# Optimization experiments

Hardware: AMD Instinct MI355X
Metric: run time of the kernel (lower is better)

## Reference

```python
import jax, jax.numpy as jnp
import numpy as np


def setup_inputs() -> dict:
    key = jax.random.key(0)
    k1, k2 = jax.random.split(key)
    B, N, M, D = 4, 8192, 8192, 3
    prediction = jax.random.normal(k1, (B, N, D), dtype=jnp.float32)
    target = jax.random.normal(k2, (B, M, D), dtype=jnp.float32)
    return {"prediction": prediction, "target": target}


def reference(prediction, target):
    # prediction: [B, N, 3], target: [B, M, 3] (already channels-last,
    # matching the module's transpose-if-needed behavior).
    x2 = jnp.sum(prediction * prediction, axis=-1)  # [B, N]
    y2 = jnp.sum(target * target, axis=-1)          # [B, M]
    xy = jnp.einsum('bnd,bmd->bnm', prediction, target)  # [B, N, M]
    d2 = x2[:, :, None] + y2[:, None, :] - 2.0 * xy
    d2 = jnp.maximum(d2, 0.0)  # numerical guard
    # pytorch3d chamfer_distance defaults: point_reduction='mean',
    # batch_reduction='mean' -> mean over points per direction, mean over batch,
    # then sum the two directions.
    cham_x = jnp.min(d2, axis=2).mean()  # pred -> target
    cham_y = jnp.min(d2, axis=1).mean()  # target -> pred
    return cham_x + cham_y
```

## Files before the change

kernel.cpp:

```cpp
#include <hip/hip_runtime.h>


#define BLOCK 256
#define RPT   8
#define MC    512
#define NPTS  8192
#define NCH   (NPTS / MC)
#define NB    4

__global__ __launch_bounds__(BLOCK) void chamfer_min_fused(
    const float* __restrict__ pred, const float* __restrict__ targ,
    float* __restrict__ pA,
    float* __restrict__ pB,
    double* __restrict__ acc, unsigned int* __restrict__ counter) {
    if (blockIdx.x == 0 && blockIdx.y == 0 && blockIdx.z == 0 && threadIdx.x == 0) {
        *acc = 0.0;
        *counter = 0u;
    }

    const int z   = blockIdx.z;
    const int dir = z >> 2, b = z & (NB - 1);
    const float* X = dir ? targ : pred;
    const float* Y = dir ? pred : targ;
    float* partial = dir ? pB : pA;

    __shared__ float4 ldsY[MC];
    const int mc = blockIdx.y;

    for (int p = threadIdx.x; p < MC; p += BLOCK) {
        const float* yp = Y + ((size_t)b * NPTS + (size_t)mc * MC + p) * 3;
        float yx = yp[0], yy = yp[1], yz = yp[2];
        ldsY[p] = make_float4(yx, yy, yz, fmaf(yx, yx, fmaf(yy, yy, yz * yz)));
    }
    __syncthreads();

    const int row0 = blockIdx.x * (BLOCK * RPT);
    float qx[RPT], qy[RPT], qz[RPT], x2[RPT], best[RPT];
#pragma unroll
    for (int r = 0; r < RPT; ++r) {
        int row = row0 + r * BLOCK + threadIdx.x;
        const float* xp = X + ((size_t)b * NPTS + row) * 3;
        float px = xp[0], py = xp[1], pz = xp[2];
        qx[r] = -2.0f * px;
        qy[r] = -2.0f * py;
        qz[r] = -2.0f * pz;
        x2[r] = fmaf(px, px, fmaf(py, py, pz * pz));
        best[r] = 3.0e38f;
    }

#pragma unroll 4
    for (int m = 0; m < MC; m += 2) {
        float4 T0 = ldsY[m];
        float4 T1 = ldsY[m + 1];
#pragma unroll
        for (int r = 0; r < RPT; ++r) {
            float c0 = fmaf(qx[r], T0.x, fmaf(qy[r], T0.y, fmaf(qz[r], T0.z, T0.w)));
            float c1 = fmaf(qx[r], T1.x, fmaf(qy[r], T1.y, fmaf(qz[r], T1.z, T1.w)));
            best[r] = fminf(fminf(best[r], c0), c1);
        }
    }

#pragma unroll
    for (int r = 0; r < RPT; ++r) {
        int row = row0 + r * BLOCK + threadIdx.x;
        partial[((size_t)b * NCH + mc) * NPTS + row] = fmaxf(best[r] + x2[r], 0.0f);
    }
}

__global__ __launch_bounds__(256) void chamfer_reduce(
    const float* __restrict__ pA, const float* __restrict__ pB,
    double* __restrict__ acc, unsigned int* __restrict__ counter,
    float* __restrict__ out) {
    const int g = blockIdx.x * 256 + threadIdx.x;
    const int half = NB * NPTS;
    const float* src = (g < half) ? pA : pB;
    const int gg = g & (half - 1);
    const int b = gg >> 13, r = gg & (NPTS - 1);

    float v = 3.0e38f;
#pragma unroll
    for (int c = 0; c < NCH; ++c)
        v = fminf(v, src[((size_t)b * NCH + c) * NPTS + r]);

    double d = (double)v;
    for (int off = 32; off > 0; off >>= 1) d += __shfl_down(d, off);
    __shared__ double sh[4];
    const int lane = threadIdx.x & 63, wid = threadIdx.x >> 6;
    if (lane == 0) sh[wid] = d;
    __syncthreads();

    if (threadIdx.x == 0) {
        double blocktotal = sh[0] + sh[1] + sh[2] + sh[3];
        atomicAdd(acc, blocktotal);
        __threadfence();
        unsigned int ticket = atomicAdd(counter, 1u);
        if (ticket == gridDim.x - 1) {
            __threadfence();
            double s = atomicAdd(acc, 0.0);
            out[0] = (float)(s / (double)(NB * NPTS));
        }
    }
}

extern "C" void kernel_launch(void* const* d_in, const int* in_sizes, int n_in,
                              void* d_out, int out_size, void* d_ws, size_t ws_size,
                              hipStream_t stream) {
    const float* pred = (const float*)d_in[0];
    const float* targ = (const float*)d_in[1];
    float* out = (float*)d_out;

    float* pA = (float*)d_ws;
    float* pB = pA + (size_t)NB * NCH * NPTS;
    double* acc = (double*)(pB + (size_t)NB * NCH * NPTS);
    unsigned int* counter = (unsigned int*)(acc + 1);

    dim3 g1(NPTS / (BLOCK * RPT), NCH, 2 * NB);
    chamfer_min_fused<<<g1, BLOCK, 0, stream>>>(pred, targ, pA, pB, acc, counter);

    const int nblk = 2 * NB * NPTS / 256;
    chamfer_reduce<<<nblk, 256, 0, stream>>>(pA, pB, acc, counter, out);
}
```

Before: 102.3 us.

## Replace brute-force pairwise min with z-bucketed spatial search and pruning

Drops the all-pairs distance scan and builds a z-coordinate bucket structure per point set. This takes four small kernels: min/max, histogram, scan and scatter. Each block of 128 z-sorted queries scans its home bucket, then expands outward only while the z-slab lower bound could still beat the current best distance. The aim is to cut the O(N·M) arithmetic down to a few buckets per query. In exchange it adds several serial low-occupancy launches and global atomics, and its run time now depends on how the points are distributed.

```diff
diff --git a/kernel.cpp b/kernel.cpp
--- a/kernel.cpp
+++ b/kernel.cpp
@@ -1,100 +1,176 @@
 #include <hip/hip_runtime.h>
 
 
-#define BLOCK 256
-#define RPT   8
-#define MC    512
 #define NPTS  8192
-#define NCH   (NPTS / MC)
 #define NB    4
-
-__global__ __launch_bounds__(BLOCK) void chamfer_min_fused(
+#define NBUK  64
+#define NSETS 8
+#define CAP   768
+
+typedef float v4f __attribute__((ext_vector_type(4)));
+
+__global__ __launch_bounds__(1024) void k_minmax(
     const float* __restrict__ pred, const float* __restrict__ targ,
-    float* __restrict__ pA,
-    float* __restrict__ pB,
-    double* __restrict__ acc, unsigned int* __restrict__ counter) {
-    if (blockIdx.x == 0 && blockIdx.y == 0 && blockIdx.z == 0 && threadIdx.x == 0) {
-        *acc = 0.0;
-        *counter = 0u;
-    }
-
-    const int z   = blockIdx.z;
-    const int dir = z >> 2, b = z & (NB - 1);
-    const float* X = dir ? targ : pred;
-    const float* Y = dir ? pred : targ;
-    float* partial = dir ? pB : pA;
-
-    __shared__ float4 ldsY[MC];
-    const int mc = blockIdx.y;
-
-    for (int p = threadIdx.x; p < MC; p += BLOCK) {
-        const float* yp = Y + ((size_t)b * NPTS + (size_t)mc * MC + p) * 3;
-        float yx = yp[0], yy = yp[1], yz = yp[2];
-        ldsY[p] = make_float4(yx, yy, yz, fmaf(yx, yx, fmaf(yy, yy, yz * yz)));
-    }
-    __syncthreads();
-
-    const int row0 = blockIdx.x * (BLOCK * RPT);
-    float qx[RPT], qy[RPT], qz[RPT], x2[RPT], best[RPT];
-#pragma unroll
-    for (int r = 0; r < RPT; ++r) {
-        int row = row0 + r * BLOCK + threadIdx.x;
-        const float* xp = X + ((size_t)b * NPTS + row) * 3;
-        float px = xp[0], py = xp[1], pz = xp[2];
-        qx[r] = -2.0f * px;
-        qy[r] = -2.0f * py;
-        qz[r] = -2.0f * pz;
-        x2[r] = fmaf(px, px, fmaf(py, py, pz * pz));
-        best[r] = 3.0e38f;
-    }
-
-#pragma unroll 4
-    for (int m = 0; m < MC; m += 2) {
-        float4 T0 = ldsY[m];
-        float4 T1 = ldsY[m + 1];
-#pragma unroll
-        for (int r = 0; r < RPT; ++r) {
-            float c0 = fmaf(qx[r], T0.x, fmaf(qy[r], T0.y, fmaf(qz[r], T0.z, T0.w)));
-            float c1 = fmaf(qx[r], T1.x, fmaf(qy[r], T1.y, fmaf(qz[r], T1.z, T1.w)));
-            best[r] = fminf(fminf(best[r], c0), c1);
-        }
-    }
-
-#pragma unroll
-    for (int r = 0; r < RPT; ++r) {
-        int row = row0 + r * BLOCK + threadIdx.x;
-        partial[((size_t)b * NCH + mc) * NPTS + row] = fmaxf(best[r] + x2[r], 0.0f);
-    }
-}
-
-__global__ __launch_bounds__(256) void chamfer_reduce(
-    const float* __restrict__ pA, const float* __restrict__ pB,
-    double* __restrict__ acc, unsigned int* __restrict__ counter,
-    float* __restrict__ out) {
+    float* __restrict__ minmaxz, double* __restrict__ acc,
+    unsigned int* __restrict__ counter) {
+    const int s = blockIdx.x, t = threadIdx.x;
+    if (s == 0 && t == 0) { *acc = 0.0; *counter = 0u; }
+    const float* P = ((s >> 2) ? targ : pred) + (size_t)(s & 3) * NPTS * 3;
+    float lo = 3e38f, hi = -3e38f;
+    for (int i = t; i < NPTS; i += 1024) {
+        float z = P[3 * i + 2];
+        lo = fminf(lo, z); hi = fmaxf(hi, z);
+    }
+    for (int off = 32; off > 0; off >>= 1) {
+        lo = fminf(lo, __shfl_down(lo, off));
+        hi = fmaxf(hi, __shfl_down(hi, off));
+    }
+    __shared__ float slo[16], shi[16];
+    const int lane = t & 63, w = t >> 6;
+    if (lane == 0) { slo[w] = lo; shi[w] = hi; }
+    __syncthreads();
+    if (t == 0) {
+        for (int i = 1; i < 16; ++i) { lo = fminf(lo, slo[i]); hi = fmaxf(hi, shi[i]); }
+        minmaxz[2 * s] = lo;
+        minmaxz[2 * s + 1] = hi;
+    }
+}
+
+__global__ __launch_bounds__(1024) void k_hist(
+    const float* __restrict__ pred, const float* __restrict__ targ,
+    const float* __restrict__ minmaxz, int* __restrict__ counts) {
+    const int s = blockIdx.x, t = threadIdx.x;
+    __shared__ int h[NBUK];
+    if (t < NBUK) h[t] = 0;
+    __syncthreads();
+    const float* P = ((s >> 2) ? targ : pred) + (size_t)(s & 3) * NPTS * 3;
+    const float zmin = minmaxz[2 * s];
+    const float inv = (float)NBUK / fmaxf(minmaxz[2 * s + 1] - zmin, 1e-30f);
+    for (int i = t; i < NPTS; i += 1024) {
+        int k = (int)((P[3 * i + 2] - zmin) * inv);
+        k = min(max(k, 0), NBUK - 1);
+        atomicAdd(&h[k], 1);
+    }
+    __syncthreads();
+    if (t < NBUK) counts[s * NBUK + t] = h[t];
+}
+
+__global__ __launch_bounds__(512) void k_scan(
+    const int* __restrict__ counts, int* __restrict__ bukoff,
+    int* __restrict__ cursor) {
+    const int s = threadIdx.x >> 6, lane = threadIdx.x & 63;
+    const int v = counts[s * NBUK + lane];
+    int inc = v;
+    for (int off = 1; off < 64; off <<= 1) {
+        int n = __shfl_up(inc, off);
+        if (lane >= off) inc += n;
+    }
+    bukoff[s * (NBUK + 1) + lane + 1] = inc;
+    cursor[s * NBUK + lane] = inc - v;
+    if (lane == 0) bukoff[s * (NBUK + 1)] = 0;
+}
+
+__global__ __launch_bounds__(1024) void k_scatter(
+    const float* __restrict__ pred, const float* __restrict__ targ,
+    const float* __restrict__ minmaxz, int* __restrict__ cursor,
+    v4f* __restrict__ scat) {
+    const int s = blockIdx.x, t = threadIdx.x;
+    const float* P = ((s >> 2) ? targ : pred) + (size_t)(s & 3) * NPTS * 3;
+    const float zmin = minmaxz[2 * s];
+    const float inv = (float)NBUK / fmaxf(minmaxz[2 * s + 1] - zmin, 1e-30f);
+    for (int i = t; i < NPTS; i += 1024) {
+        float x = P[3 * i], y = P[3 * i + 1], z = P[3 * i + 2];
+        int k = min(max((int)((z - zmin) * inv), 0), NBUK - 1);
+        int pos = atomicAdd(&cursor[s * NBUK + k], 1);
+        scat[(size_t)s * NPTS + pos] = (v4f){x, y, z, 0.f};
+    }
+}
+
+__global__ __launch_bounds__(256) void k_nn(
+    const v4f* __restrict__ scat, const int* __restrict__ bukoff,
+    const float* __restrict__ minmaxz, float* __restrict__ bestd) {
+    const int chunk = blockIdx.x, b = blockIdx.y, dir = blockIdx.z;
+    const int qset = dir ? (4 + b) : b;
+    const int yset = dir ? b : (4 + b);
+    const v4f* Q = scat + (size_t)qset * NPTS;
+    const v4f* Y = scat + (size_t)yset * NPTS;
+    const int* off = bukoff + yset * (NBUK + 1);
+    const float zminY = minmaxz[2 * yset];
+    const float wY = fmaxf(minmaxz[2 * yset + 1] - zminY, 1e-30f) / NBUK;
+    const float invY = 1.0f / wY;
+
+    const int t = threadIdx.x;
+    const int qi = chunk * 128 + (t & 127);
+    const int half = t >> 7;
+    const v4f q = Q[qi];
+    const float qx = q.x, qy = q.y, qz = q.z;
+    float best = 3e38f;
+
+    __shared__ v4f buf[CAP];
+    __shared__ int ks_sh;
+    if (t == 0) ks_sh = min(max((int)((qz - zminY) * invY), 0), NBUK - 1);
+    __syncthreads();
+    const int kstart = ks_sh;
+
+    auto scan_bucket = [&](int k) {
+        const int s0 = off[k], s1 = off[k + 1];
+        for (int base = s0; base < s1; base += CAP) {
+            const int n = min(CAP, s1 - base);
+            __syncthreads();
+            for (int j = t; j < n; j += 256) buf[j] = Y[base + j];
+            __syncthreads();
+            for (int j = half; j < n; j += 2) {
+                v4f c = buf[j];
+                float dx = qx - c.x, dy = qy - c.y, dz = qz - c.z;
+                float d2 = fmaf(dx, dx, fmaf(dy, dy, dz * dz));
+                best = fminf(best, d2);
+            }
+        }
+    };
+
+    scan_bucket(kstart);
+    int down = kstart - 1, up = kstart + 1;
+    while (true) {
+        bool ndown = false, nup = false;
+        if (down >= 0) {
+            float dzd = fmaxf(qz - (zminY + (float)(down + 1) * wY), 0.f);
+            ndown = dzd * dzd < best;
+        }
+        if (up < NBUK) {
+            float dzu = fmaxf((zminY + (float)up * wY) - qz, 0.f);
+            nup = dzu * dzu < best;
+        }
+        const int cd = __syncthreads_count(ndown);
+        const int cu = __syncthreads_count(nup);
+        if (cd == 0 && cu == 0) break;
+        if (cd) { scan_bucket(down); --down; }
+        if (cu) { scan_bucket(up);   ++up;  }
+    }
+
+    __shared__ float bh[128];
+    __syncthreads();
+    if (half) bh[t - 128] = best;
+    __syncthreads();
+    if (!half)
+        bestd[((size_t)dir * NB + b) * NPTS + qi] = fminf(best, bh[t]);
+}
+
+__global__ __launch_bounds__(256) void k_sum(
+    const float* __restrict__ bestd, double* __restrict__ acc,
+    unsigned int* __restrict__ counter, float* __restrict__ out) {
     const int g = blockIdx.x * 256 + threadIdx.x;
-    const int half = NB * NPTS;
-    const float* src = (g < half) ? pA : pB;
-    const int gg = g & (half - 1);
-    const int b = gg >> 13, r = gg & (NPTS - 1);
-
-    float v = 3.0e38f;
-#pragma unroll
-    for (int c = 0; c < NCH; ++c)
-        v = fminf(v, src[((size_t)b * NCH + c) * NPTS + r]);
-
-    double d = (double)v;
+    const v4f v = ((const v4f*)bestd)[g];
+    double d = (double)v.x + (double)v.y + (double)v.z + (double)v.w;
     for (int off = 32; off > 0; off >>= 1) d += __shfl_down(d, off);
     __shared__ double sh[4];
-    const int lane = threadIdx.x & 63, wid = threadIdx.x >> 6;
-    if (lane == 0) sh[wid] = d;
-    __syncthreads();
-
+    const int lane = threadIdx.x & 63, w = threadIdx.x >> 6;
+    if (lane == 0) sh[w] = d;
+    __syncthreads();
     if (threadIdx.x == 0) {
-        double blocktotal = sh[0] + sh[1] + sh[2] + sh[3];
-        atomicAdd(acc, blocktotal);
+        atomicAdd(acc, sh[0] + sh[1] + sh[2] + sh[3]);
         __threadfence();
-        unsigned int ticket = atomicAdd(counter, 1u);
-        if (ticket == gridDim.x - 1) {
+        unsigned int tk = atomicAdd(counter, 1u);
+        if (tk == gridDim.x - 1) {
             __threadfence();
             double s = atomicAdd(acc, 0.0);
             out[0] = (float)(s / (double)(NB * NPTS));
@@ -109,14 +185,19 @@
     const float* targ = (const float*)d_in[1];
     float* out = (float*)d_out;
 
-    float* pA = (float*)d_ws;
-    float* pB = pA + (size_t)NB * NCH * NPTS;
-    double* acc = (double*)(pB + (size_t)NB * NCH * NPTS);
+    v4f* scat = (v4f*)d_ws;
+    double* acc = (double*)(scat + (size_t)NSETS * NPTS);
     unsigned int* counter = (unsigned int*)(acc + 1);
-
-    dim3 g1(NPTS / (BLOCK * RPT), NCH, 2 * NB);
-    chamfer_min_fused<<<g1, BLOCK, 0, stream>>>(pred, targ, pA, pB, acc, counter);
-
-    const int nblk = 2 * NB * NPTS / 256;
-    chamfer_reduce<<<nblk, 256, 0, stream>>>(pA, pB, acc, counter, out);
-}
+    float* minmaxz = (float*)(counter + 3);
+    int* counts = (int*)(minmaxz + 2 * NSETS);
+    int* bukoff = counts + NSETS * NBUK;
+    int* cursor = bukoff + NSETS * (NBUK + 1);
+    float* bestd = (float*)(cursor + NSETS * NBUK);
+
+    k_minmax<<<NSETS, 1024, 0, stream>>>(pred, targ, minmaxz, acc, counter);
+    k_hist<<<NSETS, 1024, 0, stream>>>(pred, targ, minmaxz, counts);
+    k_scan<<<1, 512, 0, stream>>>(counts, bukoff, cursor);
+    k_scatter<<<NSETS, 1024, 0, stream>>>(pred, targ, minmaxz, cursor, scat);
+    k_nn<<<dim3(NPTS / 128, NB, 2), 256, 0, stream>>>(scat, bukoff, minmaxz, bestd);
+    k_sum<<<(2 * NB * NPTS / 4) / 256, 256, 0, stream>>>(bestd, acc, counter, out);
+}
```

Measured after the change: 298.7 us. +192.0%, slower.
